# Performance work log

Hardware: AMD Instinct MI355X
Metric: run time of the kernel (lower is better)

The kernel has to match this reference:

```python
import jax, jax.numpy as jnp
import numpy as np

B, N, NVT, HS, NZ = 512, 256, 32, 128, 64


def setup_inputs() -> dict:
    key = jax.random.key(0)
    ks = jax.random.split(key, 16)
    node_types = jax.random.randint(ks[0], (B, N), 0, NVT, dtype=jnp.int32)
    node_types = node_types.at[:, 0].set(0)      # START_TYPE
    node_types = node_types.at[:, -1].set(1)     # END_TYPE
    adj = jax.random.randint(ks[1], (B, N, N), 0, 2, dtype=jnp.int32)
    # DAG: edges only u -> v with u < v (strict upper triangular)
    tri = jnp.triu(jnp.ones((N, N), jnp.int32), k=1)
    adj = adj * tri[None, :, :]
    s = 0.05
    p = lambda k, shp: (jax.random.normal(k, shp, jnp.float32) * s)
    return {
        "node_types": node_types,
        "adj": adj,
        "W_ih": p(ks[2], (3 * HS, NVT)),   # grue_forward weight_ih
        "W_hh": p(ks[3], (3 * HS, HS)),    # grue_forward weight_hh
        "b_ih": p(ks[4], (3 * HS,)),
        "b_hh": p(ks[5], (3 * HS,)),
        "Wg": p(ks[6], (HS, NVT)),         # gate_forward linear
        "bg": p(ks[7], (HS,)),
        "Wm": p(ks[8], (HS, NVT)),         # mapper_forward (no bias)
        "W1": p(ks[9], (NZ, HS)),          # fc1 -> mu
        "b1": p(ks[10], (NZ,)),
        "W2": p(ks[11], (NZ, HS)),         # fc2 -> logvar
        "b2": p(ks[12], (NZ,)),
    }


def reference(node_types, adj, W_ih, W_hh, b_ih, b_hh, Wg, bg, Wm, W1, b1, W2, b2):
    hs = Wg.shape[0]
    # one-hot vertex types  [B, N, nvt]
    X = jax.nn.one_hot(node_types, Wg.shape[1], dtype=W_ih.dtype)
    # gated message from each vertex's TYPE (mapper has no bias -> padding contributes 0)
    gated = jax.nn.sigmoid(jnp.einsum('bnv,hv->bnh', X, Wg) + bg) \
            * jnp.einsum('bnv,hv->bnh', X, Wm)                      # [B, N, hs]
    A = adj.astype(gated.dtype)
    # predecessor aggregation: H_v = sum_{u: u->v} gated_u
    Hpre = jnp.einsum('buv,buh->bvh', A, gated)                     # [B, N, hs]
    # torch GRUCell(X_v, Hpre_v), vectorized over all vertices (no recurrence:
    # messages depend only on predecessor types)
    gi = jnp.einsum('bnv,gv->bng', X, W_ih) + b_ih                  # [B, N, 3hs]
    gh = jnp.einsum('bnh,gh->bng', Hpre, W_hh) + b_hh
    r = jax.nn.sigmoid(gi[..., :hs] + gh[..., :hs])
    z = jax.nn.sigmoid(gi[..., hs:2 * hs] + gh[..., hs:2 * hs])
    n = jnp.tanh(gi[..., 2 * hs:] + r * gh[..., 2 * hs:])
    Hv = (1.0 - z) * n + z * Hpre                                   # H_forward, [B, N, hs]
    # graph state: sum over vertices [1, N-1) (start=1, end_offset=1)
    Hg = Hv[:, 1:-1, :].sum(axis=1)                                 # [B, hs]
    mu = Hg @ W1.T + b1
    logvar = Hg @ W2.T + b2
    return (mu, logvar)
```

## Files before the change

### kernel.cpp

```cpp
#include <hip/hip_runtime.h>
#include <hip/hip_bf16.h>

#define HS 128
#define NVT 32
#define NN 256

typedef __attribute__((ext_vector_type(8))) short bf16x8;
typedef __attribute__((ext_vector_type(4))) float f32x4;

#define CNT_OFF  0
#define TABB_OFF 8388608
#define GIT_OFF  8421376

static __device__ __forceinline__ short f2bs(float f) {
    __hip_bfloat16 h = __float2bfloat16(f);
    short s; __builtin_memcpy(&s, &h, 2);
    return s;
}

__global__ void __launch_bounds__(512) build_tables(
    const float* __restrict__ W_ih, const float* __restrict__ W_hh,
    const float* __restrict__ b_ih, const float* __restrict__ b_hh,
    const float* __restrict__ Wg,   const float* __restrict__ bg,
    const float* __restrict__ Wm,
    short* __restrict__ TABB, float* __restrict__ GIT)
{
    __shared__ float G_s[HS];
    const int t = blockIdx.x;
    const int j = threadIdx.x;
    if (j < HS) {
        float x = Wg[j * NVT + t] + bg[j];
        float sg = __builtin_amdgcn_rcpf(1.f + __expf(-x));
        G_s[j] = sg * Wm[j * NVT + t];
    }
    __syncthreads();
    if (j < 384) {
        float acc = 0.f;
        for (int h = 0; h < HS; ++h) acc += G_s[h] * W_hh[j * HS + h];
        TABB[j * NVT + t] = f2bs(acc);
        float git = W_ih[j * NVT + t] + b_ih[j];
        if (j < 256) git += b_hh[j];
        GIT[t * 384 + j] = git;
    } else {
        TABB[j * NVT + t] = f2bs(G_s[j - 384]);
    }
}

__global__ void __launch_bounds__(256) count_preds(
    const int* __restrict__ node_types, const int* __restrict__ adj,
    short* __restrict__ cnt_out)
{
    __shared__ int cnt_s[NN * 33];
    __shared__ int types_s[NN];
    const int b = blockIdx.x;
    const int tid = threadIdx.x;
    for (int i = tid; i < NN * 33; i += 256) cnt_s[i] = 0;
    types_s[tid] = node_types[b * NN + tid];
    __syncthreads();

    const int* adjb = adj + (size_t)b * NN * NN;
    const int v = tid;
    #pragma unroll 5
    for (int u = 0; u < 255; ++u) {
        int a = adjb[u * NN + v];
        int t = types_s[u];
        cnt_s[v * 33 + t] += a;
    }
    __syncthreads();

    unsigned int* dst = (unsigned int*)cnt_out + (size_t)b * 4096;
    for (int i = tid; i < 4096; i += 256) {
        int vv = i >> 4, j2 = (i & 15) * 2;
        unsigned short lo = (unsigned short)f2bs((float)cnt_s[vv * 33 + j2]);
        unsigned short hi = (unsigned short)f2bs((float)cnt_s[vv * 33 + j2 + 1]);
        dst[i] = (unsigned int)lo | ((unsigned int)hi << 16);
    }
}

__global__ void __launch_bounds__(256) grue_main(
    const int* __restrict__ node_types,
    const short* __restrict__ cnt_ws, const short* __restrict__ TABB,
    const float* __restrict__ GIT,    const float* __restrict__ b_hh,
    const float* __restrict__ W1, const float* __restrict__ b1,
    const float* __restrict__ W2, const float* __restrict__ b2,
    float* __restrict__ out)
{
    __shared__ short cntA[NN * 40];
    __shared__ float ghT[16 * 388];
    __shared__ float HpT[16 * 132];
    __shared__ int   types_s[NN];
    __shared__ float hg_s[NN];

    const int b = blockIdx.x;
    const int tid = threadIdx.x;
    const int wave = tid >> 6, lane = tid & 63;
    const int quad = lane >> 4, col = lane & 15;

    types_s[tid] = node_types[b * NN + tid];
    {
        const uint4* src = (const uint4*)cnt_ws + (size_t)b * 1024 + tid * 4;
        uint4* dstl = (uint4*)cntA;
        #pragma unroll
        for (int c = 0; c < 4; ++c) dstl[tid * 5 + c] = src[c];
    }
    bf16x8 bfrag[8];
    #pragma unroll
    for (int i = 0; i < 8; ++i) {
        int jb = (i < 6) ? (wave * 96 + i * 16) : (384 + wave * 32 + (i - 6) * 16);
        bfrag[i] = *(const bf16x8*)(TABB + (jb + col) * 32 + quad * 8);
    }
    const int eh = tid & 127;
    const int esub = (tid >> 7) * 8;
    const float bhn = b_hh[256 + eh];
    float hg_acc = 0.f;
    __syncthreads();

    for (int m = 0; m < 16; ++m) {
        bf16x8 afrag = *(const bf16x8*)(cntA + (m * 16 + col) * 40 + quad * 8);
        f32x4 acc[8];
        #pragma unroll
        for (int i = 0; i < 8; ++i)
            acc[i] = __builtin_amdgcn_mfma_f32_16x16x32_bf16(
                afrag, bfrag[i], (f32x4){0.f, 0.f, 0.f, 0.f}, 0, 0, 0);
        __syncthreads();
        #pragma unroll
        for (int i = 0; i < 6; ++i) {
            int g = wave * 96 + i * 16 + col;
            #pragma unroll
            for (int r = 0; r < 4; ++r) ghT[(quad * 4 + r) * 388 + g] = acc[i][r];
        }
        #pragma unroll
        for (int i = 6; i < 8; ++i) {
            int h2 = wave * 32 + (i - 6) * 16 + col;
            #pragma unroll
            for (int r = 0; r < 4; ++r) HpT[(quad * 4 + r) * 132 + h2] = acc[i][r];
        }
        __syncthreads();
        #pragma unroll
        for (int vl8 = 0; vl8 < 8; ++vl8) {
            int vl = esub + vl8;
            int v = m * 16 + vl;
            int tv = types_s[v];
            const float* git = GIT + tv * 384 + eh;
            float gir = git[0], giz = git[128], gin = git[256];
            float ghr = ghT[vl * 388 + eh];
            float ghz = ghT[vl * 388 + 128 + eh];
            float ghn = ghT[vl * 388 + 256 + eh] + bhn;
            float hp  = HpT[vl * 132 + eh];
            float r = __builtin_amdgcn_rcpf(1.f + __expf(-(gir + ghr)));
            float z = __builtin_amdgcn_rcpf(1.f + __expf(-(giz + ghz)));
            float n = 1.f - 2.f * __builtin_amdgcn_rcpf(1.f + __expf(2.f * (gin + r * ghn)));
            float hv = (1.f - z) * n + z * hp;
            float msk = (v >= 1 && v < 255) ? 1.f : 0.f;
            hg_acc += msk * hv;
        }
    }
    hg_s[tid] = hg_acc;
    __syncthreads();
    if (tid < 128) hg_s[tid] = hg_s[tid] + hg_s[tid + 128];
    __syncthreads();
    if (tid < 128) {
        int which = tid >> 6, zz = tid & 63;
        const float* W = which ? W2 : W1;
        float acc2 = (which ? b2[zz] : b1[zz]);
        for (int h = 0; h < HS; ++h) acc2 += hg_s[h] * W[zz * HS + h];
        out[which * 32768 + b * 64 + zz] = acc2;
    }
}

extern "C" void kernel_launch(void* const* d_in, const int* in_sizes, int n_in,
                              void* d_out, int out_size, void* d_ws, size_t ws_size,
                              hipStream_t stream)
{
    const int* node_types = (const int*)d_in[0];
    const int* adj        = (const int*)d_in[1];
    const float* W_ih = (const float*)d_in[2];
    const float* W_hh = (const float*)d_in[3];
    const float* b_ih = (const float*)d_in[4];
    const float* b_hh = (const float*)d_in[5];
    const float* Wg   = (const float*)d_in[6];
    const float* bg   = (const float*)d_in[7];
    const float* Wm   = (const float*)d_in[8];
    const float* W1   = (const float*)d_in[9];
    const float* b1   = (const float*)d_in[10];
    const float* W2   = (const float*)d_in[11];
    const float* b2   = (const float*)d_in[12];

    char* ws = (char*)d_ws;
    short* cnt_ws = (short*)(ws + CNT_OFF);
    short* TABB   = (short*)(ws + TABB_OFF);
    float* GIT    = (float*)(ws + GIT_OFF);
    float* out    = (float*)d_out;

    build_tables<<<dim3(32), dim3(512), 0, stream>>>(W_ih, W_hh, b_ih, b_hh, Wg, bg, Wm, TABB, GIT);
    count_preds<<<dim3(512), dim3(256), 0, stream>>>(node_types, adj, cnt_ws);
    grue_main<<<dim3(512), dim3(256), 0, stream>>>(node_types, cnt_ws, TABB, GIT, b_hh, W1, b1, W2, b2, out);
}
```

Before: 261.7 us.

## Fuse predecessor counting into GRU kernel with register-packed counts

Merges the count_preds and grue_main kernels into one, so the per-vertex type counts never round-trip through global workspace. Counts are accumulated in eight packed 8-bit-lane registers, selected by a wave-uniform type, instead of shared-memory atomics-free adds. The GRU epilogue now works directly on the MFMA accumulator registers with a remapped gate/column layout, removing the ghT/HpT shared staging and two barriers per tile. GIT is stored as bf16 and cached in LDS. The 8-bit packed counters are safe only while each count stays at or below 255, and bf16 GIT adds rounding error.

```diff
diff --git a/kernel.cpp b/kernel.cpp
--- a/kernel.cpp
+++ b/kernel.cpp
@@ -8,14 +8,20 @@
 typedef __attribute__((ext_vector_type(8))) short bf16x8;
 typedef __attribute__((ext_vector_type(4))) float f32x4;
 
-#define CNT_OFF  0
-#define TABB_OFF 8388608
-#define GIT_OFF  8421376
+#define TABB_OFF 0
+#define GIT_OFF  32768
 
 static __device__ __forceinline__ short f2bs(float f) {
     __hip_bfloat16 h = __float2bfloat16(f);
     short s; __builtin_memcpy(&s, &h, 2);
     return s;
+}
+static __device__ __forceinline__ float bs2f(short s) {
+    __hip_bfloat16 h; __builtin_memcpy(&h, &s, 2);
+    return __bfloat162float(h);
+}
+static __device__ __forceinline__ float sigm(float x) {
+    return __builtin_amdgcn_rcpf(1.f + __expf(-x));
 }
 
 __global__ void __launch_bounds__(512) build_tables(
@@ -23,15 +29,14 @@
     const float* __restrict__ b_ih, const float* __restrict__ b_hh,
     const float* __restrict__ Wg,   const float* __restrict__ bg,
     const float* __restrict__ Wm,
-    short* __restrict__ TABB, float* __restrict__ GIT)
+    short* __restrict__ TABB, short* __restrict__ GIT)
 {
     __shared__ float G_s[HS];
     const int t = blockIdx.x;
     const int j = threadIdx.x;
     if (j < HS) {
         float x = Wg[j * NVT + t] + bg[j];
-        float sg = __builtin_amdgcn_rcpf(1.f + __expf(-x));
-        G_s[j] = sg * Wm[j * NVT + t];
+        G_s[j] = sigm(x) * Wm[j * NVT + t];
     }
     __syncthreads();
     if (j < 384) {
@@ -40,79 +45,90 @@
         TABB[j * NVT + t] = f2bs(acc);
         float git = W_ih[j * NVT + t] + b_ih[j];
         if (j < 256) git += b_hh[j];
-        GIT[t * 384 + j] = git;
+        GIT[t * 384 + j] = f2bs(git);
     } else {
         TABB[j * NVT + t] = f2bs(G_s[j - 384]);
     }
 }
 
-__global__ void __launch_bounds__(256) count_preds(
+__global__ void __launch_bounds__(256) dvae_fused(
     const int* __restrict__ node_types, const int* __restrict__ adj,
-    short* __restrict__ cnt_out)
-{
-    __shared__ int cnt_s[NN * 33];
-    __shared__ int types_s[NN];
-    const int b = blockIdx.x;
-    const int tid = threadIdx.x;
-    for (int i = tid; i < NN * 33; i += 256) cnt_s[i] = 0;
-    types_s[tid] = node_types[b * NN + tid];
-    __syncthreads();
-
-    const int* adjb = adj + (size_t)b * NN * NN;
-    const int v = tid;
-    #pragma unroll 5
-    for (int u = 0; u < 255; ++u) {
-        int a = adjb[u * NN + v];
-        int t = types_s[u];
-        cnt_s[v * 33 + t] += a;
-    }
-    __syncthreads();
-
-    unsigned int* dst = (unsigned int*)cnt_out + (size_t)b * 4096;
-    for (int i = tid; i < 4096; i += 256) {
-        int vv = i >> 4, j2 = (i & 15) * 2;
-        unsigned short lo = (unsigned short)f2bs((float)cnt_s[vv * 33 + j2]);
-        unsigned short hi = (unsigned short)f2bs((float)cnt_s[vv * 33 + j2 + 1]);
-        dst[i] = (unsigned int)lo | ((unsigned int)hi << 16);
-    }
-}
-
-__global__ void __launch_bounds__(256) grue_main(
-    const int* __restrict__ node_types,
-    const short* __restrict__ cnt_ws, const short* __restrict__ TABB,
-    const float* __restrict__ GIT,    const float* __restrict__ b_hh,
+    const short* __restrict__ TABB, const short* __restrict__ GIT,
+    const float* __restrict__ b_hh,
     const float* __restrict__ W1, const float* __restrict__ b1,
     const float* __restrict__ W2, const float* __restrict__ b2,
     float* __restrict__ out)
 {
     __shared__ short cntA[NN * 40];
-    __shared__ float ghT[16 * 388];
-    __shared__ float HpT[16 * 132];
+    __shared__ short GITs[NVT * 388];
     __shared__ int   types_s[NN];
-    __shared__ float hg_s[NN];
-
-    const int b = blockIdx.x;
-    const int tid = threadIdx.x;
+    __shared__ float hgp[4 * HS];
+    __shared__ float hg_s[HS];
+
+    const int b = blockIdx.x, tid = threadIdx.x;
     const int wave = tid >> 6, lane = tid & 63;
     const int quad = lane >> 4, col = lane & 15;
 
     types_s[tid] = node_types[b * NN + tid];
+
     {
-        const uint4* src = (const uint4*)cnt_ws + (size_t)b * 1024 + tid * 4;
-        uint4* dstl = (uint4*)cntA;
-        #pragma unroll
-        for (int c = 0; c < 4; ++c) dstl[tid * 5 + c] = src[c];
-    }
+        const unsigned* src = (const unsigned*)GIT;
+        unsigned* dst = (unsigned*)GITs;
+        #pragma unroll
+        for (int c = 0; c < 24; ++c) {
+            int i = c * 256 + tid;
+            int t = i / 192, j = i - t * 192;
+            dst[t * 194 + j] = src[i];
+        }
+    }
+
+    const int* adjb = adj + (size_t)b * NN * NN;
+    const int v = tid;
+    unsigned c0 = 0, c1 = 0, c2 = 0, c3 = 0, c4 = 0, c5 = 0, c6 = 0, c7 = 0;
+    for (int u0 = 0; u0 < NN; u0 += 32) {
+        int av[32];
+        #pragma unroll
+        for (int j = 0; j < 32; ++j) av[j] = adjb[(u0 + j) * NN + v];
+        #pragma unroll
+        for (int j = 0; j < 32; ++j) {
+            unsigned t = (unsigned)__builtin_amdgcn_readfirstlane(types_s[u0 + j]);
+            unsigned inc = ((unsigned)av[j]) << ((t & 3u) * 8u);
+            switch (t >> 2) {
+                case 0: c0 += inc; break;
+                case 1: c1 += inc; break;
+                case 2: c2 += inc; break;
+                case 3: c3 += inc; break;
+                case 4: c4 += inc; break;
+                case 5: c5 += inc; break;
+                case 6: c6 += inc; break;
+                default: c7 += inc; break;
+            }
+        }
+    }
+    {
+        unsigned cc[8] = {c0, c1, c2, c3, c4, c5, c6, c7};
+        unsigned* dst = (unsigned*)cntA;
+        #pragma unroll
+        for (int k = 0; k < 8; ++k) {
+            float f0 = (float)(cc[k] & 0xFF),         f1 = (float)((cc[k] >> 8) & 0xFF);
+            float f2 = (float)((cc[k] >> 16) & 0xFF), f3 = (float)((cc[k] >> 24) & 0xFF);
+            unsigned p0 = (unsigned)(unsigned short)f2bs(f0) | ((unsigned)(unsigned short)f2bs(f1) << 16);
+            unsigned p1 = (unsigned)(unsigned short)f2bs(f2) | ((unsigned)(unsigned short)f2bs(f3) << 16);
+            dst[v * 20 + 2 * k]     = p0;
+            dst[v * 20 + 2 * k + 1] = p1;
+        }
+    }
+
     bf16x8 bfrag[8];
     #pragma unroll
     for (int i = 0; i < 8; ++i) {
-        int jb = (i < 6) ? (wave * 96 + i * 16) : (384 + wave * 32 + (i - 6) * 16);
+        int gate = i >> 1, sub = (i & 1) * 16;
+        int jb = (gate < 3 ? gate * 128 : 384) + wave * 32 + sub;
         bfrag[i] = *(const bf16x8*)(TABB + (jb + col) * 32 + quad * 8);
     }
-    const int eh = tid & 127;
-    const int esub = (tid >> 7) * 8;
-    const float bhn = b_hh[256 + eh];
-    float hg_acc = 0.f;
+    const int h0 = wave * 32 + col;
+    const float bhn0 = b_hh[256 + h0], bhn1 = b_hh[256 + h0 + 16];
+    float hg0 = 0.f, hg1 = 0.f;
     __syncthreads();
 
     for (int m = 0; m < 16; ++m) {
@@ -122,47 +138,43 @@
         for (int i = 0; i < 8; ++i)
             acc[i] = __builtin_amdgcn_mfma_f32_16x16x32_bf16(
                 afrag, bfrag[i], (f32x4){0.f, 0.f, 0.f, 0.f}, 0, 0, 0);
-        __syncthreads();
-        #pragma unroll
-        for (int i = 0; i < 6; ++i) {
-            int g = wave * 96 + i * 16 + col;
-            #pragma unroll
-            for (int r = 0; r < 4; ++r) ghT[(quad * 4 + r) * 388 + g] = acc[i][r];
-        }
-        #pragma unroll
-        for (int i = 6; i < 8; ++i) {
-            int h2 = wave * 32 + (i - 6) * 16 + col;
-            #pragma unroll
-            for (int r = 0; r < 4; ++r) HpT[(quad * 4 + r) * 132 + h2] = acc[i][r];
-        }
-        __syncthreads();
-        #pragma unroll
-        for (int vl8 = 0; vl8 < 8; ++vl8) {
-            int vl = esub + vl8;
-            int v = m * 16 + vl;
-            int tv = types_s[v];
-            const float* git = GIT + tv * 384 + eh;
-            float gir = git[0], giz = git[128], gin = git[256];
-            float ghr = ghT[vl * 388 + eh];
-            float ghz = ghT[vl * 388 + 128 + eh];
-            float ghn = ghT[vl * 388 + 256 + eh] + bhn;
-            float hp  = HpT[vl * 132 + eh];
-            float r = __builtin_amdgcn_rcpf(1.f + __expf(-(gir + ghr)));
-            float z = __builtin_amdgcn_rcpf(1.f + __expf(-(giz + ghz)));
-            float n = 1.f - 2.f * __builtin_amdgcn_rcpf(1.f + __expf(2.f * (gin + r * ghn)));
-            float hv = (1.f - z) * n + z * hp;
-            float msk = (v >= 1 && v < 255) ? 1.f : 0.f;
-            hg_acc += msk * hv;
-        }
-    }
-    hg_s[tid] = hg_acc;
-    __syncthreads();
-    if (tid < 128) hg_s[tid] = hg_s[tid] + hg_s[tid + 128];
+        #pragma unroll
+        for (int r = 0; r < 4; ++r) {
+            int vv = m * 16 + quad * 4 + r;
+            int tv = types_s[vv];
+            float msk = (vv >= 1 && vv < NN - 1) ? 1.f : 0.f;
+            const short* g = GITs + tv * 388;
+            {
+                float gir = bs2f(g[h0]), giz = bs2f(g[128 + h0]), gin = bs2f(g[256 + h0]);
+                float rr = sigm(gir + acc[0][r]);
+                float zz = sigm(giz + acc[2][r]);
+                float x2 = gin + rr * (acc[4][r] + bhn0);
+                float nt = 1.f - 2.f * __builtin_amdgcn_rcpf(1.f + __expf(2.f * x2));
+                hg0 += msk * ((1.f - zz) * nt + zz * acc[6][r]);
+            }
+            {
+                int h1 = h0 + 16;
+                float gir = bs2f(g[h1]), giz = bs2f(g[128 + h1]), gin = bs2f(g[256 + h1]);
+                float rr = sigm(gir + acc[1][r]);
+                float zz = sigm(giz + acc[3][r]);
+                float x2 = gin + rr * (acc[5][r] + bhn1);
+                float nt = 1.f - 2.f * __builtin_amdgcn_rcpf(1.f + __expf(2.f * x2));
+                hg1 += msk * ((1.f - zz) * nt + zz * acc[7][r]);
+            }
+        }
+    }
+
+    hgp[quad * HS + h0]      = hg0;
+    hgp[quad * HS + h0 + 16] = hg1;
+    __syncthreads();
+    if (tid < HS)
+        hg_s[tid] = (hgp[tid] + hgp[HS + tid]) + (hgp[2 * HS + tid] + hgp[3 * HS + tid]);
     __syncthreads();
     if (tid < 128) {
         int which = tid >> 6, zz = tid & 63;
         const float* W = which ? W2 : W1;
-        float acc2 = (which ? b2[zz] : b1[zz]);
+        float acc2 = which ? b2[zz] : b1[zz];
+        #pragma unroll 4
         for (int h = 0; h < HS; ++h) acc2 += hg_s[h] * W[zz * HS + h];
         out[which * 32768 + b * 64 + zz] = acc2;
     }
@@ -187,12 +199,10 @@
     const float* b2   = (const float*)d_in[12];
 
     char* ws = (char*)d_ws;
-    short* cnt_ws = (short*)(ws + CNT_OFF);
-    short* TABB   = (short*)(ws + TABB_OFF);
-    float* GIT    = (float*)(ws + GIT_OFF);
-    float* out    = (float*)d_out;
+    short* TABB = (short*)(ws + TABB_OFF);
+    short* GIT  = (short*)(ws + GIT_OFF);
+    float* out  = (float*)d_out;
 
     build_tables<<<dim3(32), dim3(512), 0, stream>>>(W_ih, W_hh, b_ih, b_hh, Wg, bg, Wm, TABB, GIT);
-    count_preds<<<dim3(512), dim3(256), 0, stream>>>(node_types, adj, cnt_ws);
-    grue_main<<<dim3(512), dim3(256), 0, stream>>>(node_types, cnt_ws, TABB, GIT, b_hh, W1, b1, W2, b2, out);
-}
+    dvae_fused<<<dim3(512), dim3(256), 0, stream>>>(node_types, adj, TABB, GIT, b_hh, W1, b1, W2, b2, out);
+}
```

Result: faster. 247.8 us (-5.3%).
